# Kernel optimization log

Measured on AMD Instinct MI355X. Metric: run time of the kernel, lower is better.

## Reference

```python
import jax, jax.numpy as jnp
import numpy as np

DIM = 1024
HEADS = 16
DIM_HEAD = 64
INNER = HEADS * DIM_HEAD  # 1024
SCALE = 1.0 / DIM_HEAD ** 0.5


def setup_inputs() -> dict:
    key = jax.random.key(0)
    ks = jax.random.split(key, 5)
    x = jax.random.normal(ks[0], (4, 2048, DIM), dtype=jnp.float32)
    # nn.Linear weights stored as [out, in]; we keep [in, out] for x @ W
    Wq = jax.random.normal(ks[1], (DIM, INNER), dtype=jnp.float32) * (1.0 / np.sqrt(DIM))
    Wkv = jax.random.normal(ks[2], (DIM, 2 * INNER), dtype=jnp.float32) * (1.0 / np.sqrt(DIM))
    Wo = jax.random.normal(ks[3], (INNER, DIM), dtype=jnp.float32) * (1.0 / np.sqrt(INNER))
    bo = jax.random.normal(ks[4], (DIM,), dtype=jnp.float32) * 0.01
    return {"x": x, "Wq": Wq, "Wkv": Wkv, "Wo": Wo, "bo": bo}


def reference(x, Wq, Wkv, Wo, bo):
    b, n, _ = x.shape
    q = x @ Wq                      # [b, n, inner]
    kv = x @ Wkv                    # [b, n, 2*inner]
    k, v = jnp.split(kv, 2, axis=2)
    # 'b n (h d) -> b h n d'
    q = q.reshape(b, n, HEADS, DIM_HEAD).transpose(0, 2, 1, 3)
    k = k.reshape(b, n, HEADS, DIM_HEAD).transpose(0, 2, 1, 3)
    v = v.reshape(b, n, HEADS, DIM_HEAD).transpose(0, 2, 1, 3)
    scores = jnp.einsum('bhid,bhjd->bhij', q, k) * SCALE  # [b,h,n,n]
    attn = jax.nn.softmax(scores, axis=-1)
    out = jnp.einsum('bhij,bhjd->bhid', attn, v)          # [b,h,n,d]
    out = out.transpose(0, 2, 1, 3).reshape(b, n, INNER)  # 'b h n d -> b n (h d)'
    return out @ Wo + bo
```

## Files before the change

### kernel.cpp

```cpp
#include <hip/hip_runtime.h>
#include <hip/hip_bf16.h>

typedef unsigned short u16;
typedef unsigned int u32;
typedef __attribute__((ext_vector_type(8))) short s8v;
typedef __attribute__((ext_vector_type(4))) float f4v;
typedef __attribute__((ext_vector_type(4))) unsigned short u16x4;
typedef __attribute__((ext_vector_type(4))) unsigned int u32x4;

#define MFMA16(a,b,c) __builtin_amdgcn_mfma_f32_16x16x32_bf16((a),(b),(c),0,0,0)

#define TOKENS 8192
#define SEQ    2048
#define NH     16
#define DH     64
#define DIMK   1024
#define QPRE   0.18033688f

#if defined(__has_builtin)
#if __has_builtin(__builtin_amdgcn_exp2f)
#define EXP2(x) __builtin_amdgcn_exp2f(x)
#else
#define EXP2(x) __expf((x) * 0.69314718f)
#endif
#else
#define EXP2(x) __expf((x) * 0.69314718f)
#endif

__device__ __forceinline__ u16 f2bf(float x){
  union { float f; u32 u; } v; v.f = x;
  u32 r = v.u + 0x7FFFu + ((v.u >> 16) & 1u);
  return (u16)(r >> 16);
}

__device__ __forceinline__ void gld16(const u16* g, u16* s){
  __builtin_amdgcn_global_load_lds(
      (const __attribute__((address_space(1))) unsigned int*)(const void*)g,
      (__attribute__((address_space(3))) unsigned int*)(void*)s,
      16, 0, 0);
}

__global__ __launch_bounds__(256) void k_cast(const float* __restrict__ src,
                                              u16* __restrict__ dst){
  int i = (blockIdx.x * 256 + threadIdx.x) * 4;
  float4 v = *(const float4*)(src + i);
  u16x4 vh;
  float a[4] = {v.x, v.y, v.z, v.w};
#pragma unroll
  for (int j = 0; j < 4; j++) vh[j] = f2bf(a[j]);
  *(u16x4*)(dst + i) = vh;
}

__global__ __launch_bounds__(256) void k_transpose(const float* __restrict__ s0, int c0,
                                                   const float* __restrict__ s1, int c1,
                                                   int K, u16* __restrict__ dh){
  __shared__ float tile[64][65];
  int nb = blockIdx.x * 64, kb = blockIdx.y * 64;
  int tr = threadIdx.x >> 6, tc = threadIdx.x & 63;
#pragma unroll
  for (int i = 0; i < 16; i++){
    int k = kb + tr + i * 4, n = nb + tc;
    float v = (n < c0) ? s0[(size_t)k * c0 + n] : s1[(size_t)k * c1 + (n - c0)];
    tile[tr + i * 4][tc] = v;
  }
  __syncthreads();
#pragma unroll
  for (int i = 0; i < 16; i++){
    int nl = tr + i * 4, kl = tc;
    dh[(size_t)(nb + nl) * K + (kb + kl)] = f2bf(tile[kl][nl]);
  }
}

#define GQ_STAGE_A(buf,h,t) do{ \
  gld16(As + (size_t)(h)*131072 + (size_t)(t)*64,      &lds[(buf)*32768 + (h)*8192 + w*512]); \
  gld16(As + (size_t)(h)*131072 + (size_t)(t)*64 + 32, &lds[(buf)*32768 + (h)*8192 + 4096 + w*512]); }while(0)
#define GQ_STAGE_B(buf,h,t) do{ \
  gld16(Bs + (size_t)(h)*131072 + (size_t)(t)*64,      &lds[(buf)*32768 + 16384 + (h)*8192 + w*512]); \
  gld16(Bs + (size_t)(h)*131072 + (size_t)(t)*64 + 32, &lds[(buf)*32768 + 16384 + (h)*8192 + 4096 + w*512]); }while(0)
#define GQ_RDA(dst,buf,mh) do{ _Pragma("unroll") for (int i_ = 0; i_ < 4; i_++){ \
  dst[i_][0] = *(const s8v*)&lds[(buf)*32768 + aRB + ((mh)*4+i_)*512]; \
  dst[i_][1] = *(const s8v*)&lds[(buf)*32768 + aRB + 4096 + ((mh)*4+i_)*512]; } }while(0)
#define GQ_RDB(dst,buf,nh) do{ _Pragma("unroll") for (int j_ = 0; j_ < 2; j_++){ \
  dst[j_][0] = *(const s8v*)&lds[(buf)*32768 + bRB + ((nh)*2+j_)*512]; \
  dst[j_][1] = *(const s8v*)&lds[(buf)*32768 + bRB + 4096 + ((nh)*2+j_)*512]; } }while(0)
#define GQ_MMA(aS,bS,mh,nh) do{ __builtin_amdgcn_s_setprio(1); \
  _Pragma("unroll") for (int i_ = 0; i_ < 4; i_++) \
  _Pragma("unroll") for (int j_ = 0; j_ < 2; j_++){ \
    acc[(mh)*4+i_][(nh)*2+j_] = MFMA16(aS[i_][0], bS[j_][0], acc[(mh)*4+i_][(nh)*2+j_]); \
    acc[(mh)*4+i_][(nh)*2+j_] = MFMA16(aS[i_][1], bS[j_][1], acc[(mh)*4+i_][(nh)*2+j_]); } \
  __builtin_amdgcn_s_setprio(0); }while(0)
#define GQ_BAR() do{ asm volatile("" ::: "memory"); __builtin_amdgcn_s_barrier(); asm volatile("" ::: "memory"); }while(0)
#define GQ_VMW2() asm volatile("s_waitcnt vmcnt(2)" ::: "memory")

__global__ __launch_bounds__(512, 2) void k_gemm_qkv(
    const u16* __restrict__ A, const u16* __restrict__ B,
    u16* __restrict__ Qh, u16* __restrict__ Kh, u16* __restrict__ Vth)
{
  __shared__ u16 lds[65536];
  const int tid = threadIdx.x;
  const int w = tid >> 6, lane = tid & 63;
  const int lm = lane & 15, quad = lane >> 4;
  const int wm = w >> 2, wn = w & 3;

  const int bid = blockIdx.x;
  const int xcd = bid & 7, slot = bid >> 3;
  const int nt = slot >> 2;
  const int mloc = slot & 3;
  const int m0 = (xcd * 4 + mloc) * 256, n0 = nt * 256;

  const int srow = lane >> 2;
  const int scol = ((lane & 3) ^ (((lane >> 5) & 1) << 1)) * 8;
  const u16* As = A + (size_t)(m0 + w * 16 + srow) * DIMK + scol;
  const u16* Bs = B + (size_t)(n0 + w * 16 + srow) * DIMK + scol;

  const int swz = (lm & 8) << 1;
  const int aRB = wm * 8192 + lm * 32 + ((quad * 8) ^ swz);
  const int bRB = 16384 + (wn >> 1) * 8192 + (wn & 1) * 2048 + lm * 32 + ((quad * 8) ^ swz);

  f4v acc[8][4];
#pragma unroll
  for (int i = 0; i < 8; i++)
#pragma unroll
    for (int j = 0; j < 4; j++) acc[i][j] = (f4v){0.f, 0.f, 0.f, 0.f};

  s8v aA[4][2], aB[4][2], bA[2][2], bB[2][2];

  GQ_STAGE_A(0,0,0); GQ_STAGE_A(0,1,0); GQ_STAGE_B(0,0,0); GQ_STAGE_B(0,1,0);
  GQ_STAGE_A(1,0,1);
  GQ_VMW2(); GQ_BAR();
  GQ_RDA(aA,0,0); GQ_RDB(bA,0,0);

  for (int it = 0; it < 8; it++){
    const int t1 = 2 * it + 1;
    const int t2 = (it < 7) ? 2 * it + 2 : 15;
    const int t3 = (it < 7) ? 2 * it + 3 : 15;
    GQ_STAGE_A(1,1,t1); GQ_BAR(); GQ_RDA(aB,0,1);                 GQ_MMA(aA,bA,0,0);
    GQ_STAGE_B(1,0,t1); GQ_BAR(); GQ_RDB(bB,0,1);                 GQ_MMA(aB,bA,1,0);
    GQ_STAGE_B(1,1,t1); GQ_BAR();                                 GQ_MMA(aB,bB,1,1);
    GQ_STAGE_A(0,0,t2); GQ_VMW2(); GQ_BAR();
                                  GQ_RDA(aB,1,0); GQ_RDB(bA,1,0); GQ_MMA(aA,bB,0,1);
    GQ_STAGE_A(0,1,t2); GQ_BAR(); GQ_RDA(aA,1,1);                 GQ_MMA(aB,bA,0,0);
    GQ_STAGE_B(0,0,t2); GQ_BAR(); GQ_RDB(bB,1,1);                 GQ_MMA(aA,bA,1,0);
    GQ_STAGE_B(0,1,t2); GQ_BAR();                                 GQ_MMA(aA,bB,1,1);
    GQ_STAGE_A(1,0,t3); GQ_VMW2(); GQ_BAR();
                                  GQ_RDA(aA,0,0); GQ_RDB(bA,0,0); GQ_MMA(aB,bB,0,1);
  }

  if (nt < 8){
#pragma unroll
    for (int ig = 0; ig < 8; ig++)
#pragma unroll
      for (int jg = 0; jg < 4; jg++){
        const int gn = n0 + wn * 64 + jg * 16 + lm;
#pragma unroll
        for (int r = 0; r < 4; r++){
          const int gm = m0 + wm * 128 + ig * 16 + quad * 4 + r;
          float v = acc[ig][jg][r];
          if (gn < 1024){
            Qh[(size_t)gm * DIMK + gn] = f2bf(v * QPRE);
          } else {
            Kh[(size_t)gm * DIMK + (gn - 1024)] = f2bf(v);
          }
        }
      }
  } else {
    __syncthreads();
    u32* bnc = (u32*)lds;
#pragma unroll
    for (int igp = 0; igp < 4; igp++)
#pragma unroll
      for (int jg = 0; jg < 4; jg++){
        const int ddl = wn * 64 + jg * 16 + lm;
        const int colb = wm * 64 + igp * 16 + quad * 4;
        u32x4 p;
#pragma unroll
        for (int r = 0; r < 4; r++)
          p[r] = ((u32)f2bf(acc[2 * igp + 1][jg][r]) << 16) | (u32)f2bf(acc[2 * igp][jg][r]);
        const int col = colb ^ ((lm & 7) << 2);
        *(u32x4*)&bnc[ddl * 128 + col] = p;
      }
    __syncthreads();
    const int row = tid >> 1, half = tid & 1;
    const int df = n0 - 2048 + row;
    const int hh = df >> 6, dd = df & 63;
    const int bbat = m0 >> 11, ii0 = m0 & 2047;
    u32* Vg = (u32*)(Vth + ((size_t)(bbat * NH + hh) * DH + dd) * SEQ + ii0);
#pragma unroll
    for (int c = 0; c < 16; c++){
      const int cc = half * 16 + c;
      const int cb = (cc * 4) ^ ((row & 7) << 2);
      u32x4 q = *(const u32x4*)&bnc[row * 128 + cb];
      *(u32x4*)&Vg[cc * 4] = q;
    }
  }
}

__global__ __launch_bounds__(256) void k_gemm_op(
    const u16* __restrict__ A, const u16* __restrict__ B,
    const float* __restrict__ bias, float* __restrict__ Cf)
{
  __shared__ u16 sA[2][128*32], sB[2][128*32];
  const int tid = threadIdx.x, wave = tid >> 6, lane = tid & 63;
  const int lm = lane & 15, quad = lane >> 4;

  const int bid = blockIdx.x;
  const int xcd = bid & 7, slot = bid >> 3;
  const int nt = slot >> 3, mloc = slot & 7;
  const int m0 = (xcd * 8 + mloc) * 128, n0 = nt * 128;

  const int cof = (lane & 3) * 8;
  const int rsub = lane >> 2;

  f4v acc[4][4];
#pragma unroll
  for (int i = 0; i < 4; i++)
#pragma unroll
    for (int j = 0; j < 4; j++) acc[i][j] = (f4v){0.f, 0.f, 0.f, 0.f};

  const int wm = (wave >> 1) * 64, wn = (wave & 1) * 64;

  for (int kc = 0; kc < 16; kc++){
    int k = kc * 64;
#pragma unroll
    for (int cc = 0; cc < 2; cc++)
#pragma unroll
      for (int half = 0; half < 2; half++){
        int rb = wave * 32 + half * 16;
        gld16(A + (size_t)(m0 + rb + rsub) * DIMK + k + cc * 32 + cof, &sA[cc][rb * 32]);
        gld16(B + (size_t)(n0 + rb + rsub) * DIMK + k + cc * 32 + cof, &sB[cc][rb * 32]);
      }
    __syncthreads();

#pragma unroll
    for (int cc = 0; cc < 2; cc++){
      s8v ah[4], bh[4];
#pragma unroll
      for (int i = 0; i < 4; i++){
        ah[i] = *(const s8v*)&sA[cc][(wm + i * 16 + lm) * 32 + quad * 8];
        bh[i] = *(const s8v*)&sB[cc][(wn + i * 16 + lm) * 32 + quad * 8];
      }
#pragma unroll
      for (int i = 0; i < 4; i++)
#pragma unroll
        for (int j = 0; j < 4; j++)
          acc[i][j] = MFMA16(ah[i], bh[j], acc[i][j]);
    }
    __syncthreads();
  }

#pragma unroll
  for (int i = 0; i < 4; i++)
#pragma unroll
    for (int j = 0; j < 4; j++){
      int gn = n0 + wn + j * 16 + lm;
      float bv = bias[gn];
#pragma unroll
      for (int r = 0; r < 4; r++){
        int gm = m0 + wm + i * 16 + quad * 4 + r;
        Cf[(size_t)gm * DIMK + gn] = acc[i][j][r] + bv;
      }
    }
}

__global__ __launch_bounds__(256, 4) void k_attn(
    const u16* __restrict__ Qh, const u16* __restrict__ Kh, const u16* __restrict__ Vth,
    u16* __restrict__ Oh)
{
  __shared__ u16 sK[2*64*32];
  __shared__ u16 sV[2*64*32];
  __shared__ u16 sP[2*128*32];
  u32* sPd = (u32*)sP;

  const int bid = blockIdx.x;
  const int xcd = bid & 7, slot = bid >> 3;
  const int g = xcd * 8 + (slot >> 4);
  const int qt = slot & 15;
  const int b = g >> 4, h = g & 15;

  const int tid = threadIdx.x, wave = tid >> 6, lane = tid & 63;
  const int lm = lane & 15, quad = lane >> 4;
  const int tok0 = b * SEQ + qt * 128;
  const int rsub = lane >> 2;
  const int scof = ((lane & 3) ^ (((lane >> 5) & 1) << 1)) * 8;
  const int rsw = (lm & 8) << 1;
  const int psw = (quad & 2) << 2;

  s8v qf[2][2];
#pragma unroll
  for (int c = 0; c < 2; c++)
#pragma unroll
    for (int ifr = 0; ifr < 2; ifr++){
      size_t ga = (size_t)(tok0 + wave * 32 + ifr * 16 + lm) * DIMK + h * DH + c * 32 + quad * 8;
      qf[c][ifr] = *(const s8v*)(Qh + ga);
    }

  const f4v fz = (f4v){0.f, 0.f, 0.f, 0.f};

  float lpart[2][4];
  f4v oacc[2][4];
#pragma unroll
  for (int ifr = 0; ifr < 2; ifr++){
#pragma unroll
    for (int r = 0; r < 4; r++) lpart[ifr][r] = 0.f;
#pragma unroll
    for (int fd = 0; fd < 4; fd++) oacc[ifr][fd] = (f4v){0.f, 0.f, 0.f, 0.f};
  }

  for (int kt = 0; kt < 32; kt++){
    int j0 = kt * 64;
#pragma unroll
    for (int c = 0; c < 2; c++){
      size_t gk = (size_t)(b * SEQ + j0 + wave * 16 + rsub) * DIMK + h * DH + c * 32 + scof;
      gld16(Kh + gk, &sK[c * 2048 + wave * 512]);
      size_t gv = (size_t)((b * NH + h) * DH + wave * 16 + rsub) * SEQ + j0 + c * 32 + scof;
      gld16(Vth + gv, &sV[c * 2048 + wave * 512]);
    }
    __syncthreads();

    f4v s[2][4];
#pragma unroll
    for (int fn = 0; fn < 4; fn++){
      s8v kh0 = *(const s8v*)&sK[0 * 2048 + (fn * 16 + lm) * 32 + ((quad * 8) ^ rsw)];
      s8v kh1 = *(const s8v*)&sK[1 * 2048 + (fn * 16 + lm) * 32 + ((quad * 8) ^ rsw)];
#pragma unroll
      for (int ifr = 0; ifr < 2; ifr++){
        s[ifr][fn] = MFMA16(qf[0][ifr], kh0, fz);
        s[ifr][fn] = MFMA16(qf[1][ifr], kh1, s[ifr][fn]);
      }
    }

    s8v vreg[2][4];
#pragma unroll
    for (int c = 0; c < 2; c++)
#pragma unroll
      for (int fd = 0; fd < 4; fd++)
        vreg[c][fd] = *(const s8v*)&sV[c * 2048 + (fd * 16 + lm) * 32 + ((quad * 8) ^ rsw)];

#pragma unroll
    for (int ifr = 0; ifr < 2; ifr++){
#pragma unroll
      for (int fn = 0; fn < 4; fn++)
#pragma unroll
        for (int r = 0; r < 4; r++)
          s[ifr][fn][r] = EXP2(s[ifr][fn][r]);
      int rowb = wave * 32 + ifr * 16 + quad * 4;
#pragma unroll
      for (int r = 0; r < 4; r++)
#pragma unroll
        for (int jc = 0; jc < 2; jc++){
          union { float f; u32 u; } a0, a1;
          a0.f = s[ifr][jc * 2 + 0][r];
          a1.f = s[ifr][jc * 2 + 1][r];
          lpart[ifr][r] += a0.f + a1.f;
          sPd[jc * 2048 + (rowb + r) * 16 + (lm ^ psw)] = __builtin_amdgcn_perm(a1.u, a0.u, 0x07060302);
        }
    }

#pragma unroll
    for (int c = 0; c < 2; c++)
#pragma unroll
      for (int ifr = 0; ifr < 2; ifr++){
        s8v ph = *(const s8v*)&sP[c * 4096 + (wave * 32 + ifr * 16 + lm) * 32 + ((quad * 8) ^ rsw)];
#pragma unroll
        for (int fd = 0; fd < 4; fd++)
          oacc[ifr][fd] = MFMA16(ph, vreg[c][fd], oacc[ifr][fd]);
      }
    __syncthreads();
  }

#pragma unroll
  for (int ifr = 0; ifr < 2; ifr++){
#pragma unroll
    for (int off = 1; off < 16; off <<= 1)
#pragma unroll
      for (int r = 0; r < 4; r++)
        lpart[ifr][r] += __shfl_xor(lpart[ifr][r], off, 64);
    float inv[4];
#pragma unroll
    for (int r = 0; r < 4; r++) inv[r] = 1.f / lpart[ifr][r];
#pragma unroll
    for (int fd = 0; fd < 4; fd++){
      int dcol = h * DH + fd * 16 + lm;
#pragma unroll
      for (int r = 0; r < 4; r++){
        int tok = tok0 + wave * 32 + ifr * 16 + quad * 4 + r;
        Oh[(size_t)tok * DIMK + dcol] = f2bf(oacc[ifr][fd][r] * inv[r]);
      }
    }
  }
}

extern "C" void kernel_launch(void* const* d_in, const int* in_sizes, int n_in,
                              void* d_out, int out_size, void* d_ws, size_t ws_size,
                              hipStream_t stream) {
  const float* x   = (const float*)d_in[0];
  const float* Wq  = (const float*)d_in[1];
  const float* Wkv = (const float*)d_in[2];
  const float* Wo  = (const float*)d_in[3];
  const float* bo  = (const float*)d_in[4];
  float* out = (float*)d_out;

  char* ws = (char*)d_ws;
  size_t off = 0;
  auto alloc = [&](size_t bytes) -> u16* {
    u16* p = (u16*)(ws + off);
    off += (bytes + 255) & ~(size_t)255;
    return p;
  };
  const size_t TK2 = (size_t)TOKENS * DIMK * 2;
  u16* xh  = alloc(TK2);
  u16* Wh  = alloc((size_t)3072 * DIMK * 2);
  u16* WOh = alloc((size_t)1024 * DIMK * 2);
  u16* Qh  = alloc(TK2);
  u16* Kh  = alloc(TK2);
  u16* Vth = alloc(TK2);
  u16* Oh  = alloc(TK2);

  k_cast<<<dim3((TOKENS * DIMK) / 1024), 256, 0, stream>>>(x, xh);
  k_transpose<<<dim3(48, 16), 256, 0, stream>>>(Wq, 1024, Wkv, 2048, DIMK, Wh);
  k_transpose<<<dim3(16, 16), 256, 0, stream>>>(Wo, 1024, Wo, 1024, DIMK, WOh);
  k_gemm_qkv<<<dim3(384), 512, 0, stream>>>(xh, Wh, Qh, Kh, Vth);
  k_attn<<<dim3(16 * NH * 4), 256, 0, stream>>>(Qh, Kh, Vth, Oh);
  k_gemm_op<<<dim3(8 * 64), 256, 0, stream>>>(Oh, WOh, bo, out);
}
```

Measured before the change: 289.5 us.

## Double-buffer K/V tiles in attention and compute row sums via MFMA

The attention kernel now double-buffers K/V shared-memory tiles, prefetching the next tile while the current one is computed, and replaces __syncthreads with explicit vmcnt waits and barriers. It also computes the softmax denominator with an extra MFMA against a ones vector on the bf16 P tile, using a permuted P row layout, instead of scalar adds plus a shuffle reduction. It adds s_setprio around the MFMA sections and lowers launch bounds occupancy to 3 because shared memory grows. The denominator now sums the bf16-rounded P values rather than fp32, which slightly changes numerics. The lower occupancy may offset the gain from overlap.

```diff
diff --git a/kernel.cpp b/kernel.cpp
--- a/kernel.cpp
+++ b/kernel.cpp
@@ -262,13 +262,13 @@
     }
 }
 
-__global__ __launch_bounds__(256, 4) void k_attn(
+__global__ __launch_bounds__(256, 3) void k_attn(
     const u16* __restrict__ Qh, const u16* __restrict__ Kh, const u16* __restrict__ Vth,
     u16* __restrict__ Oh)
 {
-  __shared__ u16 sK[2*64*32];
-  __shared__ u16 sV[2*64*32];
-  __shared__ u16 sP[2*128*32];
+  __shared__ u16 sK[2*4096];
+  __shared__ u16 sV[2*4096];
+  __shared__ u16 sP[8192];
   u32* sPd = (u32*)sP;
 
   const int bid = blockIdx.x;
@@ -284,6 +284,7 @@
   const int scof = ((lane & 3) ^ (((lane >> 5) & 1) << 1)) * 8;
   const int rsw = (lm & 8) << 1;
   const int psw = (quad & 2) << 2;
+  const int plm = (lm & 0xA) | ((lm & 1) << 2) | ((lm >> 2) & 1);
 
   s8v qf[2][2];
 #pragma unroll
@@ -296,45 +297,56 @@
 
   const f4v fz = (f4v){0.f, 0.f, 0.f, 0.f};
 
-  float lpart[2][4];
+  s8v ones;
+#pragma unroll
+  for (int j = 0; j < 8; j++) ones[j] = (short)0x3F80;
+
   f4v oacc[2][4];
+  f4v lacc[2];
 #pragma unroll
   for (int ifr = 0; ifr < 2; ifr++){
-#pragma unroll
-    for (int r = 0; r < 4; r++) lpart[ifr][r] = 0.f;
+    lacc[ifr] = (f4v){0.f, 0.f, 0.f, 0.f};
 #pragma unroll
     for (int fd = 0; fd < 4; fd++) oacc[ifr][fd] = (f4v){0.f, 0.f, 0.f, 0.f};
   }
 
+#define AT_STAGE(p, t) do{ const int jb_ = (t) * 64; \
+  _Pragma("unroll") for (int c_ = 0; c_ < 2; c_++){ \
+    gld16(Kh + (size_t)(b * SEQ + jb_ + wave * 16 + rsub) * DIMK + h * DH + c_ * 32 + scof, \
+          &sK[(p) * 4096 + c_ * 2048 + wave * 512]); \
+    gld16(Vth + (size_t)((b * NH + h) * DH + wave * 16 + rsub) * SEQ + jb_ + c_ * 32 + scof, \
+          &sV[(p) * 4096 + c_ * 2048 + wave * 512]); } }while(0)
+#define AT_BAR() do{ asm volatile("" ::: "memory"); __builtin_amdgcn_s_barrier(); asm volatile("" ::: "memory"); }while(0)
+
+  AT_STAGE(0, 0);
+
   for (int kt = 0; kt < 32; kt++){
-    int j0 = kt * 64;
-#pragma unroll
-    for (int c = 0; c < 2; c++){
-      size_t gk = (size_t)(b * SEQ + j0 + wave * 16 + rsub) * DIMK + h * DH + c * 32 + scof;
-      gld16(Kh + gk, &sK[c * 2048 + wave * 512]);
-      size_t gv = (size_t)((b * NH + h) * DH + wave * 16 + rsub) * SEQ + j0 + c * 32 + scof;
-      gld16(Vth + gv, &sV[c * 2048 + wave * 512]);
-    }
-    __syncthreads();
+    const int p = kt & 1;
+    AT_STAGE(p ^ 1, (kt < 31) ? (kt + 1) : 31);
+    asm volatile("s_waitcnt vmcnt(4)" ::: "memory");
+    AT_BAR();
+    const int pb = p * 4096;
 
     f4v s[2][4];
+    __builtin_amdgcn_s_setprio(1);
 #pragma unroll
     for (int fn = 0; fn < 4; fn++){
-      s8v kh0 = *(const s8v*)&sK[0 * 2048 + (fn * 16 + lm) * 32 + ((quad * 8) ^ rsw)];
-      s8v kh1 = *(const s8v*)&sK[1 * 2048 + (fn * 16 + lm) * 32 + ((quad * 8) ^ rsw)];
+      s8v kh0 = *(const s8v*)&sK[pb + (fn * 16 + lm) * 32 + ((quad * 8) ^ rsw)];
+      s8v kh1 = *(const s8v*)&sK[pb + 2048 + (fn * 16 + lm) * 32 + ((quad * 8) ^ rsw)];
 #pragma unroll
       for (int ifr = 0; ifr < 2; ifr++){
         s[ifr][fn] = MFMA16(qf[0][ifr], kh0, fz);
         s[ifr][fn] = MFMA16(qf[1][ifr], kh1, s[ifr][fn]);
       }
     }
+    __builtin_amdgcn_s_setprio(0);
 
     s8v vreg[2][4];
 #pragma unroll
     for (int c = 0; c < 2; c++)
 #pragma unroll
       for (int fd = 0; fd < 4; fd++)
-        vreg[c][fd] = *(const s8v*)&sV[c * 2048 + (fd * 16 + lm) * 32 + ((quad * 8) ^ rsw)];
+        vreg[c][fd] = *(const s8v*)&sV[pb + c * 2048 + (fd * 16 + lm) * 32 + ((quad * 8) ^ rsw)];
 
 #pragma unroll
     for (int ifr = 0; ifr < 2; ifr++){
@@ -343,41 +355,41 @@
 #pragma unroll
         for (int r = 0; r < 4; r++)
           s[ifr][fn][r] = EXP2(s[ifr][fn][r]);
-      int rowb = wave * 32 + ifr * 16 + quad * 4;
-#pragma unroll
-      for (int r = 0; r < 4; r++)
+      const int slotb = wave * 32 + ifr * 16;
+#pragma unroll
+      for (int r = 0; r < 4; r++){
+        const int prw = slotb + (psw | ((r & 1) << 2) | (r & 2) | (quad & 1));
 #pragma unroll
         for (int jc = 0; jc < 2; jc++){
           union { float f; u32 u; } a0, a1;
           a0.f = s[ifr][jc * 2 + 0][r];
           a1.f = s[ifr][jc * 2 + 1][r];
-          lpart[ifr][r] += a0.f + a1.f;
-          sPd[jc * 2048 + (rowb + r) * 16 + (lm ^ psw)] = __builtin_amdgcn_perm(a1.u, a0.u, 0x07060302);
+          sPd[jc * 2048 + prw * 16 + (lm ^ psw)] = __builtin_amdgcn_perm(a1.u, a0.u, 0x07060302);
         }
-    }
-
-#pragma unroll
-    for (int c = 0; c < 2; c++)
+      }
+    }
+
+#pragma unroll
+    for (int c = 0; c < 2; c++){
+      __builtin_amdgcn_s_setprio(1);
 #pragma unroll
       for (int ifr = 0; ifr < 2; ifr++){
-        s8v ph = *(const s8v*)&sP[c * 4096 + (wave * 32 + ifr * 16 + lm) * 32 + ((quad * 8) ^ rsw)];
+        s8v ph = *(const s8v*)&sP[c * 4096 + (wave * 32 + ifr * 16 + plm) * 32 + ((quad * 8) ^ rsw)];
 #pragma unroll
         for (int fd = 0; fd < 4; fd++)
           oacc[ifr][fd] = MFMA16(ph, vreg[c][fd], oacc[ifr][fd]);
-      }
-    __syncthreads();
+        lacc[ifr] = MFMA16(ph, ones, lacc[ifr]);
+      }
+      __builtin_amdgcn_s_setprio(0);
+    }
+    AT_BAR();
   }
 
 #pragma unroll
   for (int ifr = 0; ifr < 2; ifr++){
-#pragma unroll
-    for (int off = 1; off < 16; off <<= 1)
-#pragma unroll
-      for (int r = 0; r < 4; r++)
-        lpart[ifr][r] += __shfl_xor(lpart[ifr][r], off, 64);
     float inv[4];
 #pragma unroll
-    for (int r = 0; r < 4; r++) inv[r] = 1.f / lpart[ifr][r];
+    for (int r = 0; r < 4; r++) inv[r] = 1.f / lacc[ifr][r];
 #pragma unroll
     for (int fd = 0; fd < 4; fd++){
       int dcol = h * DH + fd * 16 + lm;
```

New measurement: 285.4 us. No clear change (-1.4%).
